# Kernel tuning notes

Hardware: AMD Instinct MI355X
Metric: run time of the kernel (lower is better)

## Reference

```python
import jax, jax.numpy as jnp
import numpy as np

N_FREQ = 50          # n_frequencies
ENC_DIM = N_FREQ * 4 # sine encoding output dim = 200
EMB = 10             # n_embedding_dimensions
N_FRAG = 1_000_000
CELLS = 500
GENES = 500


def setup_inputs() -> dict:
    key = jax.random.key(0)
    ks = jax.random.split(key, 12)
    coordinates = jax.random.normal(ks[0], (N_FRAG, 2), jnp.float32) * 1000.0
    fragment_cellxgene_ix = jnp.sort(
        jax.random.randint(ks[1], (N_FRAG,), 0, CELLS * GENES, dtype=jnp.int32))
    # FragmentEmbedder MLP: Linear(200,10) -> Sigmoid -> Linear(10,10)
    W1 = jax.random.normal(ks[2], (ENC_DIM, EMB), jnp.float32) * 0.07
    b1 = jnp.zeros((EMB,), jnp.float32)
    W2 = jax.random.normal(ks[3], (EMB, EMB), jnp.float32) * 0.3
    b2 = jnp.zeros((EMB,), jnp.float32)
    # EmbeddingToExpression MLP: Linear(10,10) -> Sigmoid -> Linear(10,1)
    We1 = jax.random.normal(ks[4], (EMB, EMB), jnp.float32) * 0.3
    be1 = jnp.zeros((EMB,), jnp.float32)
    We2 = jax.random.normal(ks[5], (EMB, 1), jnp.float32) * 0.3
    be2 = jnp.zeros((1,), jnp.float32)
    return dict(coordinates=coordinates, fragment_cellxgene_ix=fragment_cellxgene_ix,
                cell_n=CELLS, gene_n=GENES,
                W1=W1, b1=b1, W2=W2, b2=b2, We1=We1, be1=be1, We2=We2, be2=be2)


def _sine_encode(coordinates):
    # frequencies: [1/1000**(2i/nf)]*2 for i in 1..nf, flattened -> [2*nf]
    i = jnp.arange(1, N_FREQ + 1, dtype=jnp.float32)
    freqs = jnp.repeat(1.0 / 1000.0 ** (2.0 * i / N_FREQ), 2)          # [100]
    shifts = jnp.tile(jnp.array([0.0, np.pi / 2], jnp.float32), N_FREQ)  # [100]
    # coordinates [N,2] -> [N,2,100] -> [N,400]? No: flatten(-2) over last two dims -> [N, 2*100]=[N,200]
    phase = coordinates[..., None] * freqs + shifts                     # [N,2,100]
    return jnp.sin(phase.reshape(coordinates.shape[0], -1))             # [N,200]


def reference(coordinates, fragment_cellxgene_ix, cell_n, gene_n,
              W1, b1, W2, b2, We1, be1, We2, be2):
    # fragment embedder
    enc = _sine_encode(coordinates)                       # [N, 200]
    h = jax.nn.sigmoid(enc @ W1 + b1)                     # [N, 10]
    emb = h @ W2 + b2                                     # [N, 10]
    # gene pooler: segment_sum over sorted cellxgene indices
    pooled = jax.ops.segment_sum(emb, fragment_cellxgene_ix,
                                 num_segments=cell_n * gene_n,
                                 indices_are_sorted=True)  # [cell*gene, 10]
    cg = pooled.reshape(cell_n, gene_n, -1)                # [cells, genes, 10]
    # embedding to expression
    h2 = jax.nn.sigmoid(cg @ We1 + be1)                    # [cells, genes, 10]
    out = (h2 @ We2 + be2)[..., 0]                         # [cells, genes]
    return out
```

## Files before the change

kernel.cpp:

```cpp
#include <hip/hip_runtime.h>
#include <hip/hip_bf16.h>

#define NFREQ 50
#define EMBD  10

typedef __attribute__((ext_vector_type(8))) short short8;
typedef __attribute__((ext_vector_type(4))) float f32x4;

__device__ __forceinline__ unsigned short bf16b(float x) {
    union { __hip_bfloat16 b; unsigned short u; } c;
    c.b = __float2bfloat16(x);
    return c.u;
}

__device__ __forceinline__ unsigned int pack_bf16_rhu(float lo, float hi) {
    union { float f; unsigned int u; } a, b;
    a.f = lo; b.f = hi;
    return __builtin_amdgcn_perm(b.u + 0x8000u, a.u + 0x8000u, 0x07060302u);
}

__device__ const float C_TAB[7][4] = {
    {7.58577575029184e-1f, 5.75439937337157e-1f, 4.36515832240166e-1f, 3.31131121482591e-1f},
    {9.12010839355910e-3f, 6.91830970918936e-3f, 5.24807460249773e-3f, 3.98107170553497e-3f},
    {1.09647819614318e-4f, 8.31763771102671e-5f, 6.30957344480193e-5f, 4.78630092322638e-5f},
    {1.31825673855641e-6f, 1.00000000000000e-6f, 7.58577575029184e-7f, 5.75439937337157e-7f},
    {1.58489319246111e-8f, 1.20226443461741e-8f, 9.12010839355910e-9f, 6.91830970918936e-9f},
    {1.90546071796325e-10f,1.44543977074593e-10f,1.09647819614318e-10f,8.31763771102671e-11f},
    {2.29086765276777e-12f,1.73780082874938e-12f,1.31825673855641e-12f,1.00000000000000e-12f}
};

__device__ __forceinline__ constexpr bool lin_slot(int kt, int p) {
    return (kt == 2 && p >= 1) || (kt == 5 && p == 3) || (kt == 6);
}

__global__ void zero_ws(float4* p, int n4) {
    int t = blockIdx.x * blockDim.x + threadIdx.x;
    float4 z = make_float4(0.f, 0.f, 0.f, 0.f);
    for (int i = t; i < n4; i += gridDim.x * blockDim.x) p[i] = z;
}

__global__ __launch_bounds__(256) void frag_kernel(
    const float2* __restrict__ coords, const int* __restrict__ cgix,
    const float* __restrict__ W1, const float* __restrict__ b1,
    const float* __restrict__ W2, const float* __restrict__ b2,
    float* __restrict__ pooled, int n)
{
    __shared__ unsigned short w1lds[7 * 4 * 16 * 8];
    __shared__ float hbufT[4][10][68];

    const int tid  = threadIdx.x;
    const int wid  = tid >> 6;
    const int lane = tid & 63;
    const int grp  = lane >> 4;
    const int col  = lane & 15;
    const int t = blockIdx.x * 256 + tid;
    const bool active = t < n;

    int seg = active ? cgix[t] : -1;

    float2 cxy[4];
    #pragma unroll
    for (int s = 0; s < 4; ++s) {
        int rt = blockIdx.x * 256 + wid * 64 + s * 16 + col;
        cxy[s] = (rt < n) ? coords[rt] : make_float2(0.f, 0.f);
    }

    #pragma unroll
    for (int it = 0; it < 14; ++it) {
        int idx = it * 256 + tid;
        int e = idx & 7, c = (idx >> 3) & 15, g = (idx >> 7) & 3, kt = idx >> 9;
        int k = kt * 32 + g * 8 + e;
        float w = (k < 2 * NFREQ * 2 && c < EMBD) ? W1[k * EMBD + c] : 0.f;
        w1lds[idx] = bf16b(w);
    }
    __syncthreads();

    short8 Bf[7];
    #pragma unroll
    for (int kt = 0; kt < 7; ++kt)
        Bf[kt] = *reinterpret_cast<const short8*>(&w1lds[((kt * 4 + grp) * 16 + col) * 8]);

    float G = (grp == 0) ? 1.0f
            : (grp == 1) ? 3.31131121482591e-1f
            : (grp == 2) ? 1.09647819614318e-1f
                         : 3.63078054770101e-2f;
    float gi = G * 0.15915494309189535f;
    float gy = gi * 1.0e6f;

    float b1v = (col < EMBD) ? b1[col] : 0.f;

    #pragma unroll
    for (int s = 0; s < 4; ++s) {
        float ax  = cxy[s].x * gi;
        float ay  = cxy[s].y * gy;
        float a01 = (grp == 0) ? ax : ay;
        f32x4 acc = {b1v, b1v, b1v, b1v};
        #pragma unroll
        for (int kt = 0; kt < 7; ++kt) {
            union { short8 s8; unsigned int u[4]; } a;
            #pragma unroll
            for (int p = 0; p < 4; ++p) {
                float base;
                if      (kt < 3) base = ax;
                else if (kt > 3) base = ay;
                else             base = (p < 2) ? a01 : ay;
                float sv, cv;
                if (lin_slot(kt, p)) {
                    float phi = base * (C_TAB[kt][p] * 6.28318530717958647f);
                    float t2  = phi * phi;
                    sv = phi * fmaf(t2, -0.16666666666f, 1.0f);
                    cv = fmaf(t2, -0.5f, 1.0f);
                } else {
                    float rr = __builtin_amdgcn_fractf(base * C_TAB[kt][p]);
                    sv = __builtin_amdgcn_sinf(rr);
                    cv = __builtin_amdgcn_cosf(rr);
                }
                a.u[p] = pack_bf16_rhu(sv, cv);
            }
            acc = __builtin_amdgcn_mfma_f32_16x16x32_bf16(a.s8, Bf[kt], acc, 0, 0, 0);
        }
        if (col < EMBD)
            *reinterpret_cast<f32x4*>(&hbufT[wid][col][s * 16 + grp * 4]) = acc;
    }
    asm volatile("s_waitcnt lgkmcnt(0)" ::: "memory");
    __builtin_amdgcn_sched_barrier(0);

    float h[EMBD];
    #pragma unroll
    for (int j = 0; j < EMBD; ++j) {
        float a = hbufT[wid][j][lane];
        h[j] = __builtin_amdgcn_rcpf(1.0f + __expf(-a));
    }
    float e[EMBD];
    #pragma unroll
    for (int j = 0; j < EMBD; ++j) e[j] = b2[j];
    #pragma unroll
    for (int m = 0; m < EMBD; ++m) {
        #pragma unroll
        for (int j = 0; j < EMBD; ++j) e[j] = fmaf(h[m], W2[m * EMBD + j], e[j]);
    }

    for (int d = 1; d < 64; d <<= 1) {
        int sup = __shfl_up(seg, d, 64);
        bool ok = (lane >= d) && (sup == seg);
        if (__builtin_amdgcn_ballot_w64(ok) == 0ull) break;
        #pragma unroll
        for (int j = 0; j < EMBD; ++j) {
            float u = __shfl_up(e[j], d, 64);
            e[j] += ok ? u : 0.0f;
        }
    }

    int seg_next = __shfl_down(seg, 1, 64);
    bool writer = active && ((lane == 63) || (seg_next != seg));
    int first_seg = __shfl(seg, 0, 64);
    int last_seg  = __shfl(seg, 63, 64);

    if (writer) {
        float* p = pooled + (long)seg * EMBD;
        if (seg == first_seg || seg == last_seg) {
            #pragma unroll
            for (int j = 0; j < EMBD; ++j) unsafeAtomicAdd(p + j, e[j]);
        } else {
            #pragma unroll
            for (int j = 0; j < EMBD; ++j) p[j] = e[j];
        }
    }
}

__global__ __launch_bounds__(256) void expr_kernel(
    const float* __restrict__ pooled,
    const float* __restrict__ We1, const float* __restrict__ be1,
    const float* __restrict__ We2, const float* __restrict__ be2,
    float* __restrict__ out, int nseg)
{
    int t = blockIdx.x * blockDim.x + threadIdx.x;
    if (t >= nseg) return;
    const float2* p2 = (const float2*)(pooled + (long)t * EMBD);
    float x[EMBD];
    #pragma unroll
    for (int j = 0; j < EMBD / 2; ++j) {
        float2 v = p2[j];
        x[2*j] = v.x; x[2*j+1] = v.y;
    }
    float o = be2[0];
    #pragma unroll
    for (int j = 0; j < EMBD; ++j) {
        float a = be1[j];
        #pragma unroll
        for (int m = 0; m < EMBD; ++m) a = fmaf(x[m], We1[m * EMBD + j], a);
        float hj = __builtin_amdgcn_rcpf(1.0f + __expf(-a));
        o = fmaf(hj, We2[j], o);
    }
    out[t] = o;
}

extern "C" void kernel_launch(void* const* d_in, const int* in_sizes, int n_in,
                              void* d_out, int out_size, void* d_ws, size_t ws_size,
                              hipStream_t stream) {
    const float2* coords = (const float2*)d_in[0];
    const int*    cgix   = (const int*)d_in[1];
    const float*  W1     = (const float*)d_in[4];
    const float*  b1     = (const float*)d_in[5];
    const float*  W2     = (const float*)d_in[6];
    const float*  b2     = (const float*)d_in[7];
    const float*  We1    = (const float*)d_in[8];
    const float*  be1    = (const float*)d_in[9];
    const float*  We2    = (const float*)d_in[10];
    const float*  be2    = (const float*)d_in[11];
    float*        out    = (float*)d_out;

    int n    = in_sizes[0] / 2;
    int nseg = out_size;
    float* pooled = (float*)d_ws;

    int n4 = (nseg * EMBD) / 4;
    int zb = (n4 + 255) / 256;
    zero_ws<<<zb, 256, 0, stream>>>((float4*)pooled, n4);

    frag_kernel<<<(n + 255) / 256, 256, 0, stream>>>(coords, cgix, W1, b1, W2, b2,
                                                     pooled, n);
    expr_kernel<<<(nseg + 255) / 256, 256, 0, stream>>>(pooled, We1, be1, We2, be2,
                                                        out, nseg);
}
```

Baseline: 58.52 us.

## Process two tiles per block with prefetch of next tile's inputs

```diff
diff --git a/kernel.cpp b/kernel.cpp
--- a/kernel.cpp
+++ b/kernel.cpp
@@ -7,10 +7,9 @@
 typedef __attribute__((ext_vector_type(8))) short short8;
 typedef __attribute__((ext_vector_type(4))) float f32x4;
 
-__device__ __forceinline__ unsigned short bf16b(float x) {
-    union { __hip_bfloat16 b; unsigned short u; } c;
-    c.b = __float2bfloat16(x);
-    return c.u;
+__device__ __forceinline__ unsigned short bf16_rhu(float x) {
+    union { float f; unsigned u; } c; c.f = x;
+    return (unsigned short)((c.u + 0x8000u) >> 16);
 }
 
 __device__ __forceinline__ unsigned int pack_bf16_rhu(float lo, float hi) {
@@ -43,7 +42,7 @@
     const float2* __restrict__ coords, const int* __restrict__ cgix,
     const float* __restrict__ W1, const float* __restrict__ b1,
     const float* __restrict__ W2, const float* __restrict__ b2,
-    float* __restrict__ pooled, int n)
+    float* __restrict__ pooled, int n, int tstride)
 {
     __shared__ unsigned short w1lds[7 * 4 * 16 * 8];
     __shared__ float hbufT[4][10][68];
@@ -53,17 +52,6 @@
     const int lane = tid & 63;
     const int grp  = lane >> 4;
     const int col  = lane & 15;
-    const int t = blockIdx.x * 256 + tid;
-    const bool active = t < n;
-
-    int seg = active ? cgix[t] : -1;
-
-    float2 cxy[4];
-    #pragma unroll
-    for (int s = 0; s < 4; ++s) {
-        int rt = blockIdx.x * 256 + wid * 64 + s * 16 + col;
-        cxy[s] = (rt < n) ? coords[rt] : make_float2(0.f, 0.f);
-    }
 
     #pragma unroll
     for (int it = 0; it < 14; ++it) {
@@ -71,8 +59,15 @@
         int e = idx & 7, c = (idx >> 3) & 15, g = (idx >> 7) & 3, kt = idx >> 9;
         int k = kt * 32 + g * 8 + e;
         float w = (k < 2 * NFREQ * 2 && c < EMBD) ? W1[k * EMBD + c] : 0.f;
-        w1lds[idx] = bf16b(w);
-    }
+        w1lds[idx] = bf16_rhu(w);
+    }
+
+    int tile = blockIdx.x;
+    int t0 = tile * 256 + tid;
+    bool act = t0 < n;
+    int   seg = act ? cgix[t0] : -1;
+    float2 cc = act ? coords[t0] : make_float2(0.f, 0.f);
+
     __syncthreads();
 
     short8 Bf[7];
@@ -86,85 +81,104 @@
                          : 3.63078054770101e-2f;
     float gi = G * 0.15915494309189535f;
     float gy = gi * 1.0e6f;
-
     float b1v = (col < EMBD) ? b1[col] : 0.f;
 
     #pragma unroll
-    for (int s = 0; s < 4; ++s) {
-        float ax  = cxy[s].x * gi;
-        float ay  = cxy[s].y * gy;
-        float a01 = (grp == 0) ? ax : ay;
-        f32x4 acc = {b1v, b1v, b1v, b1v};
-        #pragma unroll
-        for (int kt = 0; kt < 7; ++kt) {
-            union { short8 s8; unsigned int u[4]; } a;
+    for (int itr = 0; itr < 2; ++itr) {
+        int   seg2 = -1;
+        float2 cc2 = make_float2(0.f, 0.f);
+        if (itr == 0) {
+            int t2 = (tile + tstride) * 256 + tid;
+            bool a2 = t2 < n;
+            seg2 = a2 ? cgix[t2] : -1;
+            cc2  = a2 ? coords[t2] : make_float2(0.f, 0.f);
+        }
+
+        #pragma unroll
+        for (int s = 0; s < 4; ++s) {
+            float cx = __shfl(cc.x, s * 16 + col, 64);
+            float cy = __shfl(cc.y, s * 16 + col, 64);
+            float ax  = cx * gi;
+            float ay  = cy * gy;
+            float a01 = (grp == 0) ? ax : ay;
+            f32x4 acc = {b1v, b1v, b1v, b1v};
             #pragma unroll
-            for (int p = 0; p < 4; ++p) {
-                float base;
-                if      (kt < 3) base = ax;
-                else if (kt > 3) base = ay;
-                else             base = (p < 2) ? a01 : ay;
-                float sv, cv;
-                if (lin_slot(kt, p)) {
-                    float phi = base * (C_TAB[kt][p] * 6.28318530717958647f);
-                    float t2  = phi * phi;
-                    sv = phi * fmaf(t2, -0.16666666666f, 1.0f);
-                    cv = fmaf(t2, -0.5f, 1.0f);
-                } else {
-                    float rr = __builtin_amdgcn_fractf(base * C_TAB[kt][p]);
-                    sv = __builtin_amdgcn_sinf(rr);
-                    cv = __builtin_amdgcn_cosf(rr);
+            for (int kt = 0; kt < 7; ++kt) {
+                union { short8 s8; unsigned int u[4]; } a;
+                #pragma unroll
+                for (int p = 0; p < 4; ++p) {
+                    float base;
+                    if      (kt < 3) base = ax;
+                    else if (kt > 3) base = ay;
+                    else             base = (p < 2) ? a01 : ay;
+                    float sv, cv;
+                    if (lin_slot(kt, p)) {
+                        float phi = base * (C_TAB[kt][p] * 6.28318530717958647f);
+                        float t2v = phi * phi;
+                        sv = phi * fmaf(t2v, -0.16666666666f, 1.0f);
+                        cv = fmaf(t2v, -0.5f, 1.0f);
+                    } else {
+                        float rr = __builtin_amdgcn_fractf(base * C_TAB[kt][p]);
+                        sv = __builtin_amdgcn_sinf(rr);
+                        cv = __builtin_amdgcn_cosf(rr);
+                    }
+                    a.u[p] = pack_bf16_rhu(sv, cv);
                 }
-                a.u[p] = pack_bf16_rhu(sv, cv);
+                acc = __builtin_amdgcn_mfma_f32_16x16x32_bf16(a.s8, Bf[kt], acc, 0, 0, 0);
             }
-            acc = __builtin_amdgcn_mfma_f32_16x16x32_bf16(a.s8, Bf[kt], acc, 0, 0, 0);
-        }
-        if (col < EMBD)
-            *reinterpret_cast<f32x4*>(&hbufT[wid][col][s * 16 + grp * 4]) = acc;
-    }
-    asm volatile("s_waitcnt lgkmcnt(0)" ::: "memory");
-    __builtin_amdgcn_sched_barrier(0);
-
-    float h[EMBD];
-    #pragma unroll
-    for (int j = 0; j < EMBD; ++j) {
-        float a = hbufT[wid][j][lane];
-        h[j] = __builtin_amdgcn_rcpf(1.0f + __expf(-a));
-    }
-    float e[EMBD];
-    #pragma unroll
-    for (int j = 0; j < EMBD; ++j) e[j] = b2[j];
-    #pragma unroll
-    for (int m = 0; m < EMBD; ++m) {
-        #pragma unroll
-        for (int j = 0; j < EMBD; ++j) e[j] = fmaf(h[m], W2[m * EMBD + j], e[j]);
-    }
-
-    for (int d = 1; d < 64; d <<= 1) {
-        int sup = __shfl_up(seg, d, 64);
-        bool ok = (lane >= d) && (sup == seg);
-        if (__builtin_amdgcn_ballot_w64(ok) == 0ull) break;
+            if (col < EMBD)
+                *reinterpret_cast<f32x4*>(&hbufT[wid][col][s * 16 + grp * 4]) = acc;
+        }
+        asm volatile("s_waitcnt lgkmcnt(0)" ::: "memory");
+        __builtin_amdgcn_sched_barrier(0);
+
+        float h[EMBD];
         #pragma unroll
         for (int j = 0; j < EMBD; ++j) {
-            float u = __shfl_up(e[j], d, 64);
-            e[j] += ok ? u : 0.0f;
-        }
-    }
-
-    int seg_next = __shfl_down(seg, 1, 64);
-    bool writer = active && ((lane == 63) || (seg_next != seg));
-    int first_seg = __shfl(seg, 0, 64);
-    int last_seg  = __shfl(seg, 63, 64);
-
-    if (writer) {
-        float* p = pooled + (long)seg * EMBD;
-        if (seg == first_seg || seg == last_seg) {
+            float aa = hbufT[wid][j][lane];
+            h[j] = __builtin_amdgcn_rcpf(1.0f + __expf(-aa));
+        }
+        float e[EMBD];
+        #pragma unroll
+        for (int j = 0; j < EMBD; ++j) e[j] = b2[j];
+        #pragma unroll
+        for (int m = 0; m < EMBD; ++m) {
             #pragma unroll
-            for (int j = 0; j < EMBD; ++j) unsafeAtomicAdd(p + j, e[j]);
-        } else {
+            for (int j = 0; j < EMBD; ++j) e[j] = fmaf(h[m], W2[m * EMBD + j], e[j]);
+        }
+
+        for (int d = 1; d < 64; d <<= 1) {
+            int sup = __shfl_up(seg, d, 64);
+            bool ok = (lane >= d) && (sup == seg);
+            if (__builtin_amdgcn_ballot_w64(ok) == 0ull) break;
             #pragma unroll
-            for (int j = 0; j < EMBD; ++j) p[j] = e[j];
-        }
+            for (int j = 0; j < EMBD; ++j) {
+                float u = __shfl_up(e[j], d, 64);
+                e[j] += ok ? u : 0.0f;
+            }
+        }
+
+        int seg_next = __shfl_down(seg, 1, 64);
+        bool writer = act && ((lane == 63) || (seg_next != seg));
+        int first_seg = __shfl(seg, 0, 64);
+        int last_seg  = __shfl(seg, 63, 64);
+
+        if (writer) {
+            float* p = pooled + (long)seg * EMBD;
+            if (seg == first_seg || seg == last_seg) {
+                #pragma unroll
+                for (int j = 0; j < EMBD; ++j) unsafeAtomicAdd(p + j, e[j]);
+            } else {
+                #pragma unroll
+                for (int j = 0; j < EMBD; ++j) p[j] = e[j];
+            }
+        }
+
+        tile += tstride;
+        if (tile * 256 >= n) break;
+        act = (tile * 256 + tid) < n;
+        seg = seg2;
+        cc  = cc2;
     }
 }
 
@@ -218,8 +232,10 @@
     int zb = (n4 + 255) / 256;
     zero_ws<<<zb, 256, 0, stream>>>((float4*)pooled, n4);
 
-    frag_kernel<<<(n + 255) / 256, 256, 0, stream>>>(coords, cgix, W1, b1, W2, b2,
-                                                     pooled, n);
+    int ntiles  = (n + 255) / 256;
+    int tstride = (ntiles + 1) / 2;
+    frag_kernel<<<tstride, 256, 0, stream>>>(coords, cgix, W1, b1, W2, b2,
+                                             pooled, n, tstride);
     expr_kernel<<<(nseg + 255) / 256, 256, 0, stream>>>(pooled, We1, be1, We2, be2,
                                                         out, nseg);
 }
```

Result: no change. 57.90 us (-1.1%).
